# Kernel optimization log

Measured on AMD Instinct MI355X. Metric: run time of the kernel, lower is better.

Reference implementation:

```python
import jax, jax.numpy as jnp
from jax import lax
import numpy as np

B = 4096        # num_batch
NVAR = 120      # 3 * num_legs(4) * horizon(10)
NC = 2 * NVAR   # num_constraints = 240
HID = 1024      # GRU hidden size
RIN = 3 * (NC + NVAR)  # GRU input dim = 1080
MAXITER = 8
RHO = 1.0
REG = 1e-4


def setup_inputs() -> dict:
    key = jax.random.key(0)
    ks = jax.random.split(key, 10)
    # SPD quadratic cost H, linear cost g, inequality constraints C x <= c
    M = jax.random.normal(ks[0], (NVAR, NVAR), jnp.float32)
    H = M @ M.T / NVAR + jnp.eye(NVAR, dtype=jnp.float32)
    g = jax.random.normal(ks[1], (NVAR,), jnp.float32)
    C = 0.1 * jax.random.normal(ks[2], (NC, NVAR), jnp.float32)
    c = jax.random.uniform(ks[3], (NC,), jnp.float32, 0.1, 1.0)
    lamda_init = jax.random.normal(ks[4], (B, NVAR), jnp.float32)
    s_init = jax.random.uniform(ks[5], (B, NC), jnp.float32)
    h_0 = jnp.zeros((B, HID), jnp.float32)
    # GRU cell (torch GRUCell layout: [3*HID, in]) + output head to NC+NVAR
    sc_i = 1.0 / np.sqrt(RIN)
    sc_h = 1.0 / np.sqrt(HID)
    W_ih = sc_i * jax.random.normal(ks[6], (3 * HID, RIN), jnp.float32)
    b_ih = jnp.zeros((3 * HID,), jnp.float32)
    W_hh = sc_h * jax.random.normal(ks[7], (3 * HID, HID), jnp.float32)
    b_hh = jnp.zeros((3 * HID,), jnp.float32)
    W_out = sc_h * jax.random.normal(ks[8], (NC + NVAR, HID), jnp.float32)
    b_out = jnp.zeros((NC + NVAR,), jnp.float32)
    return dict(lamda_init=lamda_init, s_init=s_init, h_0=h_0, H=H, g=g, C=C, c=c,
                W_ih=W_ih, b_ih=b_ih, W_hh=W_hh, b_hh=b_hh, W_out=W_out, b_out=b_out)


def _gru_cell(x, h, W_ih, b_ih, W_hh, b_hh):
    gi = x @ W_ih.T + b_ih
    gh = h @ W_hh.T + b_hh
    i_r, i_z, i_n = jnp.split(gi, 3, axis=1)
    h_r, h_z, h_n = jnp.split(gh, 3, axis=1)
    r = jax.nn.sigmoid(i_r + h_r)
    z = jax.nn.sigmoid(i_z + h_z)
    n = jnp.tanh(i_n + r * h_n)
    return (1.0 - z) * n + z * h


def reference(lamda_init, s_init, h_0, H, g, C, c, W_ih, b_ih, W_hh, b_hh, W_out, b_out):
    I = jnp.eye(NVAR, dtype=H.dtype)
    # ---- init solve (compute_projection_gru preamble) ----
    Q_inv0 = jnp.linalg.pinv(H + REG * I)
    lincost0 = -0.0 * lamda_init + g                 # [B, NVAR]
    xi0 = (-lincost0) @ Q_inv0.T                     # sol = (Qinv @ rhs.T).T
    s0 = jnp.maximum(0.0, -(xi0 @ C.T) + c)
    s0 = 0.0 * s_init + s0                           # s_init = 0*nn + 1*s_
    lam0 = lamda_init
    # ---- constant per-iteration projection matrix (same every iter) ----
    Q_inv = jnp.linalg.pinv(H + RHO * (C.T @ C) + REG * I)

    def step(carry, _):
        s, lam, h = carry
        # compute_feasible_control
        b_aug = c - s                                # [B, NC]
        lincost = -lam + g - RHO * (b_aug @ C)       # [B, NVAR]
        xi = (-lincost) @ Q_inv.T                    # [B, NVAR]
        Axi = xi @ C.T                               # [B, NC]
        s_new = jnp.maximum(0.0, -Axi + c)
        res_vec = Axi - c + s_new
        res_norm = jnp.linalg.norm(res_vec, axis=1)
        lam_new = lam - RHO * (res_vec @ C)
        qp_cost = 0.5 * (xi @ H @ xi.T) + xi @ g     # [B, B] (faithful to source)
        qp_norm = jnp.linalg.norm(qp_cost, axis=1)
        # GRU refinement
        r = jnp.concatenate([s, lam, s_new, lam_new, s_new - s, lam_new - lam], axis=1)
        h_new = _gru_cell(r, h, W_ih, b_ih, W_hh, b_hh)
        out = h_new @ W_out.T + b_out                # [B, NC+NVAR]
        s_fin = jnp.maximum(0.0, s_new + out[:, :NC])
        lam_fin = lam_new + out[:, NC:NC + NVAR]
        fixed = jnp.linalg.norm(lam - lam_fin, axis=1) + jnp.linalg.norm(s - s_fin, axis=1)
        return (s_fin, lam_fin, h_new), (xi, res_norm, fixed, qp_norm)

    (_, _, _), (xis, primal, fixed, qpres) = lax.scan(step, (s0, lam0, h_0), None, length=MAXITER)
    return xis[-1], primal, fixed, qpres
```

## Files before the change

kernel.cpp:

```cpp
#include <hip/hip_runtime.h>
#include <hip/hip_bf16.h>
#include <math.h>

#define NB    4096
#define NV    120
#define NCN   240
#define HIDD  1024
#define RINN  1080
#define NOUTD 360
#define NOUTP 384
#define NITER 8
#define REGEPS 1e-4f
#define NPART 512

#define KCAT 4224
#define HOFF 2176
#define KWC  2112
#define KWO  1024
#define NSTEP_R 34
#define NSTEPS  66

typedef unsigned short u16;
typedef __attribute__((ext_vector_type(8))) short short8v;
typedef __attribute__((ext_vector_type(4))) float f32x4;

__device__ inline u16 f2b(float x) {
    __hip_bfloat16 h = __float2bfloat16(x);
    return __builtin_bit_cast(u16, h);
}
__device__ inline float b2f(u16 u) {
    __hip_bfloat16 h = __builtin_bit_cast(__hip_bfloat16, u);
    return __bfloat162float(h);
}

__device__ inline void gl16(const void* g, void* l) {
    __builtin_amdgcn_global_load_lds(
        (__attribute__((address_space(1))) void*)(void*)g,
        (__attribute__((address_space(3))) void*)l, 16, 0, 0);
}

__global__ void k_buildA(const float* __restrict__ H, const float* __restrict__ C,
                         float* __restrict__ A, float* __restrict__ A0) {
    int i = blockIdx.x;
    int which = blockIdx.y;
    for (int j = threadIdx.x; j < NV; j += blockDim.x) {
        float v = H[i*NV + j] + (i == j ? REGEPS : 0.f);
        if (which == 0) {
            float acc = 0.f;
            for (int k = 0; k < NCN; ++k) acc += C[k*NV + i] * C[k*NV + j];
            A[i*NV + j] = v + acc;
        } else {
            A0[i*NV + j] = v;
        }
    }
}

__global__ void k_buildCT(const float* __restrict__ C, float* __restrict__ CT) {
    int j = blockIdx.x;
    for (int k = threadIdx.x; k < NCN; k += 256)
        CT[(size_t)j * NCN + k] = C[(size_t)k * NV + j];
}

__device__ inline void inv4x4(const float* m, float* inv) {
    float s0 = m[0]*m[5] - m[1]*m[4];
    float s1 = m[0]*m[6] - m[2]*m[4];
    float s2 = m[0]*m[7] - m[3]*m[4];
    float s3 = m[1]*m[6] - m[2]*m[5];
    float s4 = m[1]*m[7] - m[3]*m[5];
    float s5 = m[2]*m[7] - m[3]*m[6];
    float c5 = m[10]*m[15] - m[11]*m[14];
    float c4 = m[9]*m[15] - m[11]*m[13];
    float c3 = m[9]*m[14] - m[10]*m[13];
    float c2 = m[8]*m[15] - m[11]*m[12];
    float c1 = m[8]*m[14] - m[10]*m[12];
    float c0 = m[8]*m[13] - m[9]*m[12];
    float det = s0*c5 - s1*c4 + s2*c3 + s3*c2 - s4*c1 + s5*c0;
    float id = 1.0f / det;
    inv[0]  = ( m[5]*c5 - m[6]*c4 + m[7]*c3) * id;
    inv[1]  = (-m[1]*c5 + m[2]*c4 - m[3]*c3) * id;
    inv[2]  = ( m[13]*s5 - m[14]*s4 + m[15]*s3) * id;
    inv[3]  = (-m[9]*s5 + m[10]*s4 - m[11]*s3) * id;
    inv[4]  = (-m[4]*c5 + m[6]*c2 - m[7]*c1) * id;
    inv[5]  = ( m[0]*c5 - m[2]*c2 + m[3]*c1) * id;
    inv[6]  = (-m[12]*s5 + m[14]*s2 - m[15]*s1) * id;
    inv[7]  = ( m[8]*s5 - m[10]*s2 + m[11]*s1) * id;
    inv[8]  = ( m[4]*c4 - m[5]*c2 + m[7]*c0) * id;
    inv[9]  = (-m[0]*c4 + m[1]*c2 - m[3]*c0) * id;
    inv[10] = ( m[12]*s4 - m[13]*s2 + m[15]*s0) * id;
    inv[11] = (-m[8]*s4 + m[9]*s2 - m[11]*s0) * id;
    inv[12] = (-m[4]*c3 + m[5]*c1 - m[6]*c0) * id;
    inv[13] = ( m[0]*c3 - m[1]*c1 + m[2]*c0) * id;
    inv[14] = (-m[12]*s3 + m[13]*s1 - m[14]*s0) * id;
    inv[15] = ( m[8]*s3 - m[9]*s1 + m[10]*s0) * id;
}

__global__ __launch_bounds__(1024) void k_invert(const float* __restrict__ Ain,
                                                 const float* __restrict__ A0in,
                                                 float* __restrict__ Qi,
                                                 float* __restrict__ Qi0) {
    __shared__ float M[NV][132];
    __shared__ float Rl[4][132];
    __shared__ float Bl[16];
    const float* src = (blockIdx.x == 0) ? Ain : A0in;
    float* dst = (blockIdx.x == 0) ? Qi : Qi0;
    const int t = threadIdx.x;
    for (int idx = t; idx < NV*132; idx += 1024) {
        int i = idx / 132, j = idx - i*132;
        M[i][j] = (j < NV) ? src[i*NV + j] : 0.f;
    }
    __syncthreads();
    const int ty = t >> 5;
    const int g4 = (t & 31) * 4;
    for (int kk = 0; kk < NV; kk += 4) {
        if (ty == 0) {
            float a[16], b[16];
            #pragma unroll
            for (int p = 0; p < 4; ++p) {
                float4 v = *(const float4*)&M[kk + p][kk];
                a[p*4+0] = v.x; a[p*4+1] = v.y; a[p*4+2] = v.z; a[p*4+3] = v.w;
            }
            inv4x4(a, b);
            float4 m0v = *(const float4*)&M[kk+0][g4];
            float4 m1v = *(const float4*)&M[kk+1][g4];
            float4 m2v = *(const float4*)&M[kk+2][g4];
            float4 m3v = *(const float4*)&M[kk+3][g4];
            #pragma unroll
            for (int p = 0; p < 4; ++p) {
                float4 r;
                r.x = b[p*4+0]*m0v.x + b[p*4+1]*m1v.x + b[p*4+2]*m2v.x + b[p*4+3]*m3v.x;
                r.y = b[p*4+0]*m0v.y + b[p*4+1]*m1v.y + b[p*4+2]*m2v.y + b[p*4+3]*m3v.y;
                r.z = b[p*4+0]*m0v.z + b[p*4+1]*m1v.z + b[p*4+2]*m2v.z + b[p*4+3]*m3v.z;
                r.w = b[p*4+0]*m0v.w + b[p*4+1]*m1v.w + b[p*4+2]*m2v.w + b[p*4+3]*m3v.w;
                *(float4*)&Rl[p][g4] = r;
            }
            if (t < 16) Bl[t] = b[t];
        }
        float4 F[4];
        #pragma unroll
        for (int q = 0; q < 4; ++q) {
            int i = ty + 32*q;
            F[q] = (i < NV) ? *(const float4*)&M[i][kk] : float4{0.f,0.f,0.f,0.f};
        }
        __syncthreads();
        #pragma unroll
        for (int q = 0; q < 4; ++q) {
            int i = ty + 32*q;
            if (i < NV) {
                int dp = i - kk;
                bool ispiv = (dp >= 0) && (dp < 4);
                float4 v;
                if (g4 == kk) {
                    if (ispiv) {
                        v = *(const float4*)&Bl[dp*4];
                    } else {
                        v.x = -(F[q].x*Bl[0] + F[q].y*Bl[4] + F[q].z*Bl[8]  + F[q].w*Bl[12]);
                        v.y = -(F[q].x*Bl[1] + F[q].y*Bl[5] + F[q].z*Bl[9]  + F[q].w*Bl[13]);
                        v.z = -(F[q].x*Bl[2] + F[q].y*Bl[6] + F[q].z*Bl[10] + F[q].w*Bl[14]);
                        v.w = -(F[q].x*Bl[3] + F[q].y*Bl[7] + F[q].z*Bl[11] + F[q].w*Bl[15]);
                    }
                } else if (ispiv) {
                    v = *(const float4*)&Rl[dp][g4];
                } else {
                    float4 r0 = *(const float4*)&Rl[0][g4];
                    float4 r1 = *(const float4*)&Rl[1][g4];
                    float4 r2 = *(const float4*)&Rl[2][g4];
                    float4 r3 = *(const float4*)&Rl[3][g4];
                    v = *(const float4*)&M[i][g4];
                    v.x -= F[q].x*r0.x + F[q].y*r1.x + F[q].z*r2.x + F[q].w*r3.x;
                    v.y -= F[q].x*r0.y + F[q].y*r1.y + F[q].z*r2.y + F[q].w*r3.y;
                    v.z -= F[q].x*r0.z + F[q].y*r1.z + F[q].z*r2.z + F[q].w*r3.z;
                    v.w -= F[q].x*r0.w + F[q].y*r1.w + F[q].z*r2.w + F[q].w*r3.w;
                }
                *(float4*)&M[i][g4] = v;
            }
        }
        __syncthreads();
    }
    for (int idx = t; idx < NV*NV; idx += 1024) {
        int i = idx / NV, j = idx - i*NV;
        dst[idx] = M[i][j];
    }
}

__global__ void k_s0(const float* __restrict__ Qi0, const float* __restrict__ g,
                     const float* __restrict__ C, const float* __restrict__ c,
                     float* __restrict__ s0v) {
    __shared__ float xi0[NV];
    int t = threadIdx.x;
    if (t < NV) {
        float a = 0.f;
        for (int j = 0; j < NV; ++j) a += Qi0[t*NV + j] * g[j];
        xi0[t] = -a;
    }
    __syncthreads();
    if (t < NCN) {
        float a = 0.f;
        for (int j = 0; j < NV; ++j) a += C[t*NV + j] * xi0[j];
        s0v[t] = fmaxf(0.f, c[t] - a);
    }
}

__global__ void k_init(const float* __restrict__ s0v, const float* __restrict__ lam0,
                       float* __restrict__ s, float* __restrict__ lam) {
    int b0 = blockIdx.x * 8;
    int t = threadIdx.x;
    for (int idx = t; idx < 8*NCN; idx += 256) {
        int m = idx / NCN, k = idx % NCN;
        s[(size_t)(b0 + m)*NCN + k] = s0v[k];
    }
    for (int idx = t; idx < 8*NV; idx += 256) lam[(size_t)b0*NV + idx] = lam0[(size_t)b0*NV + idx];
}

__global__ void k_packH(const float* __restrict__ h0, u16* __restrict__ act) {
    int n = blockIdx.x;
    size_t base = (size_t)n * KCAT + HOFF;
    for (int k = threadIdx.x; k < HIDD; k += 256) {
        float x = h0[(size_t)n * HIDD + k];
        u16 hi = f2b(x);
        act[base + k] = hi;
        act[base + HIDD + k] = f2b(x - b2f(hi));
    }
}

__global__ void k_packWcat(const float* __restrict__ Wih, const float* __restrict__ Whh,
                           u16* __restrict__ Wc) {
    int n = blockIdx.x;
    size_t base = (size_t)n * KWC;
    for (int k = threadIdx.x; k < 1088; k += 256)
        Wc[base + k] = f2b(k < RINN ? Wih[(size_t)n * RINN + k] : 0.f);
    for (int k = threadIdx.x; k < HIDD; k += 256)
        Wc[base + 1088 + k] = f2b(Whh[(size_t)n * HIDD + k]);
}

__global__ void k_packWo(const float* __restrict__ src, u16* __restrict__ dst) {
    int n = blockIdx.x;
    size_t row = (size_t)n * KWO;
    for (int k = threadIdx.x; k < KWO; k += 256)
        dst[row + k] = f2b(n < NOUTD ? src[(size_t)n * HIDD + k] : 0.f);
}

__device__ inline void write2(u16* __restrict__ act, size_t base, int pos, float x) {
    u16 hi = f2b(x);
    u16 lo = f2b(x - b2f(hi));
    act[base + pos] = hi;
    act[base + 1088 + pos] = lo;
}

__device__ inline float hadd4(float4 v) { return (v.x + v.y) + (v.z + v.w); }

#define XB 8
__global__ __launch_bounds__(512) void k_xiproj(
        const float* __restrict__ s, const float* __restrict__ lam,
        const float* __restrict__ Cg, const float* __restrict__ CTg,
        const float* __restrict__ c,
        const float* __restrict__ g, const float* __restrict__ Qi,
        const float* __restrict__ Hg,
        float* __restrict__ xi, float* __restrict__ Y,
        float* __restrict__ snew, float* __restrict__ lamn,
        u16* __restrict__ act, float* __restrict__ primal,
        double* __restrict__ Gp, double* __restrict__ vp, double* __restrict__ Sp) {
    __shared__ float Msh[31680];
    __shared__ float bd[XB][NCN];
    __shared__ float ul[XB][NV];
    __shared__ float xl[XB][NV];
    __shared__ float resl[XB][NCN];
    __shared__ float wl[XB];
    const int b0 = blockIdx.x * XB;
    const int t = threadIdx.x;

    for (int idx = t; idx < XB*NCN; idx += 512) {
        int m = idx / NCN, k = idx - m*NCN;
        bd[m][k] = c[k] - s[(size_t)(b0 + m)*NCN + k];
    }
    for (int idx = t; idx < NV*NCN; idx += 512) {
        int i = idx / NCN, k = idx - i*NCN;
        Msh[i*244 + k] = CTg[idx];
    }
    __syncthreads();
    if (t < 240) {
        int m = t / 30, jb = t - (t / 30) * 30;
        float4 a0 = {0,0,0,0}, a1 = {0,0,0,0}, a2 = {0,0,0,0}, a3 = {0,0,0,0};
        for (int kg = 0; kg < 60; ++kg) {
            float4 b4 = *(const float4*)&bd[m][kg*4];
            float4 c0 = *(const float4*)&Msh[(jb     ) * 244 + kg*4];
            float4 c1 = *(const float4*)&Msh[(jb + 30) * 244 + kg*4];
            float4 c2 = *(const float4*)&Msh[(jb + 60) * 244 + kg*4];
            float4 c3 = *(const float4*)&Msh[(jb + 90) * 244 + kg*4];
            a0.x += b4.x*c0.x; a0.y += b4.y*c0.y; a0.z += b4.z*c0.z; a0.w += b4.w*c0.w;
            a1.x += b4.x*c1.x; a1.y += b4.y*c1.y; a1.z += b4.z*c1.z; a1.w += b4.w*c1.w;
            a2.x += b4.x*c2.x; a2.y += b4.y*c2.y; a2.z += b4.z*c2.z; a2.w += b4.w*c2.w;
            a3.x += b4.x*c3.x; a3.y += b4.y*c3.y; a3.z += b4.z*c3.z; a3.w += b4.w*c3.w;
        }
        #pragma unroll
        for (int p = 0; p < 4; ++p) {
            int j = jb + 30*p;
            float h = (p == 0) ? hadd4(a0) : (p == 1) ? hadd4(a1) : (p == 2) ? hadd4(a2) : hadd4(a3);
            ul[m][j] = lam[(size_t)(b0 + m)*NV + j] - g[j] + h;
        }
    }
    __syncthreads();
    for (int idx = t; idx < NV*NV; idx += 512) {
        int i = idx / NV, j = idx - i*NV;
        Msh[i*132 + j] = Qi[idx];
        Msh[(120 + i)*132 + j] = Hg[idx];
    }
    __syncthreads();
    if (t < 240) {
        int m = t / 30, ib = t - (t / 30) * 30;
        float4 a0 = {0,0,0,0}, a1 = {0,0,0,0}, a2 = {0,0,0,0}, a3 = {0,0,0,0};
        for (int jg = 0; jg < 30; ++jg) {
            float4 u4 = *(const float4*)&ul[m][jg*4];
            float4 q0 = *(const float4*)&Msh[(ib     ) * 132 + jg*4];
            float4 q1 = *(const float4*)&Msh[(ib + 30) * 132 + jg*4];
            float4 q2 = *(const float4*)&Msh[(ib + 60) * 132 + jg*4];
            float4 q3 = *(const float4*)&Msh[(ib + 90) * 132 + jg*4];
            a0.x += u4.x*q0.x; a0.y += u4.y*q0.y; a0.z += u4.z*q0.z; a0.w += u4.w*q0.w;
            a1.x += u4.x*q1.x; a1.y += u4.y*q1.y; a1.z += u4.z*q1.z; a1.w += u4.w*q1.w;
            a2.x += u4.x*q2.x; a2.y += u4.y*q2.y; a2.z += u4.z*q2.z; a2.w += u4.w*q2.w;
            a3.x += u4.x*q3.x; a3.y += u4.y*q3.y; a3.z += u4.z*q3.z; a3.w += u4.w*q3.w;
        }
        #pragma unroll
        for (int p = 0; p < 4; ++p) {
            int i = ib + 30*p;
            float a = (p == 0) ? hadd4(a0) : (p == 1) ? hadd4(a1) : (p == 2) ? hadd4(a2) : hadd4(a3);
            xl[m][i] = a;
            xi[(size_t)(b0 + m)*NV + i] = a;
        }
    }
    __syncthreads();
    if (t < 240) {
        int m = t / 30, ib = t - (t / 30) * 30;
        float4 a0 = {0,0,0,0}, a1 = {0,0,0,0}, a2 = {0,0,0,0}, a3 = {0,0,0,0};
        for (int jg = 0; jg < 30; ++jg) {
            float4 x4 = *(const float4*)&xl[m][jg*4];
            float4 h0 = *(const float4*)&Msh[(120 + ib     ) * 132 + jg*4];
            float4 h1 = *(const float4*)&Msh[(120 + ib + 30) * 132 + jg*4];
            float4 h2 = *(const float4*)&Msh[(120 + ib + 60) * 132 + jg*4];
            float4 h3 = *(const float4*)&Msh[(120 + ib + 90) * 132 + jg*4];
            a0.x += x4.x*h0.x; a0.y += x4.y*h0.y; a0.z += x4.z*h0.z; a0.w += x4.w*h0.w;
            a1.x += x4.x*h1.x; a1.y += x4.y*h1.y; a1.z += x4.z*h1.z; a1.w += x4.w*h1.w;
            a2.x += x4.x*h2.x; a2.y += x4.y*h2.y; a2.z += x4.z*h2.z; a2.w += x4.w*h2.w;
            a3.x += x4.x*h3.x; a3.y += x4.y*h3.y; a3.z += x4.z*h3.z; a3.w += x4.w*h3.w;
        }
        #pragma unroll
        for (int p = 0; p < 4; ++p) {
            int i = ib + 30*p;
            float a = (p == 0) ? hadd4(a0) : (p == 1) ? hadd4(a1) : (p == 2) ? hadd4(a2) : hadd4(a3);
            Y[(size_t)(b0 + m)*NV + i] = a;
        }
    }
    if (t >= 240 && t < 240 + XB) {
        int m = t - 240;
        float a = 0.f;
        for (int j = 0; j < NV; ++j) a += xl[m][j] * g[j];
        wl[m] = a;
    }
    __syncthreads();
    for (int idx = t; idx < NCN*NV; idx += 512) {
        int k = idx / NV, j = idx - k*NV;
        Msh[k*132 + j] = Cg[idx];
    }
    __syncthreads();
    if (t < 480) {
        int m = t / 60, kb = t - (t / 60) * 60;
        float4 a0 = {0,0,0,0}, a1 = {0,0,0,0}, a2 = {0,0,0,0}, a3 = {0,0,0,0};
        for (int jg = 0; jg < 30; ++jg) {
            float4 x4 = *(const float4*)&xl[m][jg*4];
            float4 c0 = *(const float4*)&Msh[(kb      ) * 132 + jg*4];
            float4 c1 = *(const float4*)&Msh[(kb + 60 ) * 132 + jg*4];
            float4 c2 = *(const float4*)&Msh[(kb + 120) * 132 + jg*4];
            float4 c3 = *(const float4*)&Msh[(kb + 180) * 132 + jg*4];
            a0.x += x4.x*c0.x; a0.y += x4.y*c0.y; a0.z += x4.z*c0.z; a0.w += x4.w*c0.w;
            a1.x += x4.x*c1.x; a1.y += x4.y*c1.y; a1.z += x4.z*c1.z; a1.w += x4.w*c1.w;
            a2.x += x4.x*c2.x; a2.y += x4.y*c2.y; a2.z += x4.z*c2.z; a2.w += x4.w*c2.w;
            a3.x += x4.x*c3.x; a3.y += x4.y*c3.y; a3.z += x4.z*c3.z; a3.w += x4.w*c3.w;
        }
        #pragma unroll
        for (int p = 0; p < 4; ++p) {
            int k = kb + 60*p;
            float a = (p == 0) ? hadd4(a0) : (p == 1) ? hadd4(a1) : (p == 2) ? hadd4(a2) : hadd4(a3);
            float sn = fmaxf(0.f, c[k] - a);
            float rv = a - c[k] + sn;
            resl[m][k] = rv;
            int b = b0 + m;
            snew[(size_t)b*NCN + k] = sn;
            float so = s[(size_t)b*NCN + k];
            size_t base = (size_t)b * KCAT;
            write2(act, base, k, so);
            write2(act, base, 360 + k, sn);
            write2(act, base, 720 + k, sn - so);
        }
    }
    __syncthreads();
    if (t < XB) {
        float a = 0.f;
        for (int k = 0; k < NCN; ++k) a += resl[t][k] * resl[t][k];
        primal[b0 + t] = sqrtf(a);
    }
    for (int idx = t; idx < NV*NCN; idx += 512) {
        int i = idx / NCN, k = idx - i*NCN;
        Msh[i*244 + k] = CTg[idx];
    }
    __syncthreads();
    if (t < 240) {
        int m = t / 30, ib = t - (t / 30) * 30;
        float4 a0 = {0,0,0,0}, a1 = {0,0,0,0}, a2 = {0,0,0,0}, a3 = {0,0,0,0};
        for (int kg = 0; kg < 60; ++kg) {
            float4 r4 = *(const float4*)&resl[m][kg*4];
            float4 c0 = *(const float4*)&Msh[(ib     ) * 244 + kg*4];
            float4 c1 = *(const float4*)&Msh[(ib + 30) * 244 + kg*4];
            float4 c2 = *(const float4*)&Msh[(ib + 60) * 244 + kg*4];
            float4 c3 = *(const float4*)&Msh[(ib + 90) * 244 + kg*4];
            a0.x += r4.x*c0.x; a0.y += r4.y*c0.y; a0.z += r4.z*c0.z; a0.w += r4.w*c0.w;
            a1.x += r4.x*c1.x; a1.y += r4.y*c1.y; a1.z += r4.z*c1.z; a1.w += r4.w*c1.w;
            a2.x += r4.x*c2.x; a2.y += r4.y*c2.y; a2.z += r4.z*c2.z; a2.w += r4.w*c2.w;
            a3.x += r4.x*c3.x; a3.y += r4.y*c3.y; a3.z += r4.z*c3.z; a3.w += r4.w*c3.w;
        }
        #pragma unroll
        for (int p = 0; p < 4; ++p) {
            int i = ib + 30*p;
            float a = (p == 0) ? hadd4(a0) : (p == 1) ? hadd4(a1) : (p == 2) ? hadd4(a2) : hadd4(a3);
            int b = b0 + m;
            float lo = lam[(size_t)b*NV + i];
            float ln = lo - a;
            lamn[(size_t)b*NV + i] = ln;
            size_t base = (size_t)b * KCAT;
            write2(act, base, 240 + i, lo);
            write2(act, base, 600 + i, ln);
            write2(act, base, 960 + i, ln - lo);
        }
    }
    for (int idx = t; idx < XB*8; idx += 512) {
        int m = idx >> 3, k = 1080 + (idx & 7);
        size_t base = (size_t)(b0 + m) * KCAT;
        act[base + k] = 0;
        act[base + 1088 + k] = 0;
    }
    for (int idx = t; idx < NV*NV; idx += 512) {
        int i = idx / NV, j = idx - i*NV;
        double a = 0.0;
        #pragma unroll
        for (int m = 0; m < XB; ++m) a += (double)xl[m][i] * (double)xl[m][j];
        Gp[(size_t)blockIdx.x*NV*NV + idx] = a;
    }
    if (t < NV) {
        double a = 0.0;
        #pragma unroll
        for (int m = 0; m < XB; ++m) a += (double)wl[m] * (double)xl[m][t];
        vp[(size_t)blockIdx.x*NV + t] = a;
    }
    if (t == 0) {
        double a = 0.0;
        #pragma unroll
        for (int m = 0; m < XB; ++m) a += (double)wl[m] * (double)wl[m];
        Sp[blockIdx.x] = a;
    }
}

__global__ void k_qp_red(const double* __restrict__ Gp, const double* __restrict__ vp,
                         const double* __restrict__ Sp,
                         double* __restrict__ G, double* __restrict__ v, double* __restrict__ S) {
    int idx = blockIdx.x * 256 + threadIdx.x;
    if (idx < NV*NV) {
        double a = 0.0;
        for (int p = 0; p < NPART; ++p) a += Gp[(size_t)p*NV*NV + idx];
        G[idx] = a;
    }
    if (idx < NV) {
        double a = 0.0;
        for (int p = 0; p < NPART; ++p) a += vp[(size_t)p*NV + idx];
        v[idx] = a;
    }
    if (idx == 0) {
        double a = 0.0;
        for (int p = 0; p < NPART; ++p) a += Sp[p];
        S[0] = a;
    }
}

__global__ __launch_bounds__(256) void k_tail(
        const float* __restrict__ Yb, const double* __restrict__ G,
        const double* __restrict__ v, const double* __restrict__ S,
        float* __restrict__ qp,
        const float* __restrict__ snew, const float* __restrict__ lamn,
        const float* __restrict__ outb,
        float* __restrict__ s, float* __restrict__ lam,
        float* __restrict__ fx) {
    __shared__ float Yl[16][NV];
    __shared__ double tl[16][NV];
    __shared__ float redS[16][17];
    __shared__ float redL[16][17];
    int b0 = blockIdx.x * 16;
    int t = threadIdx.x;
    for (int idx = t; idx < 16*NV; idx += 256) Yl[idx/NV][idx%NV] = Yb[(size_t)b0*NV + idx];
    __syncthreads();
    for (int idx = t; idx < 16*NV; idx += 256) {
        int m = idx / NV, i = idx % NV;
        double a = 0.0;
        for (int j = 0; j < NV; ++j) a += G[j*NV + i] * (double)Yl[m][j];
        tl[m][i] = a;
    }
    __syncthreads();
    if (t < 16) {
        double a = 0.0, bv = 0.0;
        for (int i = 0; i < NV; ++i) { a += (double)Yl[t][i] * tl[t][i]; bv += (double)Yl[t][i] * v[i]; }
        double q = 0.25 * a + bv + S[0];
        qp[b0 + t] = (float)sqrt(q > 0.0 ? q : 0.0);
    }
    int tm = t / 16;
    int tk = t % 16;
    int b = b0 + tm;
    float ds2 = 0.f, dl2 = 0.f;
    for (int k = tk; k < NCN; k += 16) {
        float o = outb[(size_t)b*NOUTP + k];
        float sf = fmaxf(0.f, snew[(size_t)b*NCN + k] + o);
        float so = s[(size_t)b*NCN + k];
        s[(size_t)b*NCN + k] = sf;
        float d = so - sf;
        ds2 += d * d;
    }
    for (int i = tk; i < NV; i += 16) {
        float o = outb[(size_t)b*NOUTP + NCN + i];
        float lf = lamn[(size_t)b*NV + i] + o;
        float lo = lam[(size_t)b*NV + i];
        lam[(size_t)b*NV + i] = lf;
        float d = lo - lf;
        dl2 += d * d;
    }
    redS[tm][tk] = ds2;
    redL[tm][tk] = dl2;
    __syncthreads();
    if (tk == 0) {
        float a = 0.f, l = 0.f;
        for (int q = 0; q < 16; ++q) { a += redS[tm][q]; l += redL[tm][q]; }
        fx[b] = sqrtf(l) + sqrtf(a);
    }
}

#define GRUF_STEP(NSLOT, BUFI) do {                                              \
    char* Ah_ = lds + (BUFI) * 32768;                                            \
    char* Al_ = Ah_ + 4096;                                                      \
    char* Bb_ = Ah_ + 8192;                                                      \
    const int srow = lane & 15;                                                  \
    const int ksl = lane >> 4;                                                   \
    short8v ah[2], al[2];                                                        \
    _Pragma("unroll")                                                            \
    for (int fm = 0; fm < 2; ++fm) {                                             \
        int rr = wm * 32 + fm * 16 + srow;                                       \
        int off = rr * 64 + ((ksl ^ ((rr >> 1) & 3)) << 4);                      \
        ah[fm] = *(const short8v*)(Ah_ + off);                                   \
        al[fm] = *(const short8v*)(Al_ + off);                                   \
    }                                                                            \
    _Pragma("unroll")                                                            \
    for (int fn = 0; fn < 2; ++fn) {                                             \
        int rb = wn * 32 + fn * 16 + srow;                                       \
        int boff = rb * 64 + ((ksl ^ ((rb >> 1) & 3)) << 4);                     \
        short8v bfr = *(const short8v*)(Bb_ + boff);                             \
        short8v bfz = *(const short8v*)(Bb_ + 8192 + boff);                      \
        short8v bfn = *(const short8v*)(Bb_ + 16384 + boff);                     \
        _Pragma("unroll")                                                        \
        for (int fm = 0; fm < 2; ++fm) {                                         \
            acc[0][fn][fm] = __builtin_amdgcn_mfma_f32_16x16x32_bf16(ah[fm], bfr, acc[0][fn][fm], 0, 0, 0); \
            acc[0][fn][fm] = __builtin_amdgcn_mfma_f32_16x16x32_bf16(al[fm], bfr, acc[0][fn][fm], 0, 0, 0); \
            acc[1][fn][fm] = __builtin_amdgcn_mfma_f32_16x16x32_bf16(ah[fm], bfz, acc[1][fn][fm], 0, 0, 0); \
            acc[1][fn][fm] = __builtin_amdgcn_mfma_f32_16x16x32_bf16(al[fm], bfz, acc[1][fn][fm], 0, 0, 0); \
            acc[NSLOT][fn][fm] = __builtin_amdgcn_mfma_f32_16x16x32_bf16(ah[fm], bfn, acc[NSLOT][fn][fm], 0, 0, 0); \
            acc[NSLOT][fn][fm] = __builtin_amdgcn_mfma_f32_16x16x32_bf16(al[fm], bfn, acc[NSLOT][fn][fm], 0, 0, 0); \
        }                                                                        \
    }                                                                            \
} while (0)

__global__ __launch_bounds__(512) void k_gruf(
        const u16* __restrict__ act,
        const u16* __restrict__ Wc,
        const float* __restrict__ bih, const float* __restrict__ bhh,
        u16* __restrict__ actn) {
    __shared__ char lds[65536];
    const int t = threadIdx.x;
    const int lane = t & 63;
    const int wid = t >> 6;
    const int wm = wid >> 2;
    const int wn = wid & 3;
    const int bid = blockIdx.x;
    const int xcd = bid & 7;
    const int slot = bid >> 3;
    const int m0 = (xcd * 8 + (slot & 7)) * 64;
    const int n0 = (slot >> 3) * 128;

    f32x4 acc[4][2][2];
    #pragma unroll
    for (int i = 0; i < 4; ++i)
        #pragma unroll
        for (int j = 0; j < 2; ++j)
            #pragma unroll
            for (int k = 0; k < 2; ++k) {
                f32x4 z = {0.f, 0.f, 0.f, 0.f};
                acc[i][j][k] = z;
            }

    auto stage = [&](int step, int buf) {
        char* Ah_ = lds + buf * 32768;
        char* Al_ = Ah_ + 4096;
        char* Bb_ = Ah_ + 8192;
        const int hiOff = (step < NSTEP_R) ? step * 32 : step * 32 + 1088;
        const int loOff = hiOff + ((step < NSTEP_R) ? 1088 : 1024);
        const int wOff = step * 32;
        {
            int rr = (wid & 3) * 16 + (lane >> 2);
            int kq = ((lane & 3) ^ ((rr >> 1) & 3)) << 3;
            if (wid < 4)
                gl16(act + (size_t)(m0 + rr) * KCAT + hiOff + kq, Ah_ + (wid & 3) * 1024);
            else
                gl16(act + (size_t)(m0 + rr) * KCAT + loOff + kq, Al_ + (wid & 3) * 1024);
        }
        #pragma unroll
        for (int j = 0; j < 3; ++j) {
            int cb = wid * 3 + j;
            int rbg = cb * 16 + (lane >> 2);
            int kq = ((lane & 3) ^ ((rbg >> 1) & 3)) << 3;
            gl16(Wc + (size_t)((rbg >> 7) * 1024 + n0 + (rbg & 127)) * KWC + wOff + kq,
                 Bb_ + cb * 1024);
        }
    };

    stage(0, 0);
    __syncthreads();
    int cur = 0;
    for (int step = 0; step < NSTEP_R; ++step) {
        stage(step + 1, cur ^ 1);
        GRUF_STEP(2, cur);
        __syncthreads();
        cur ^= 1;
    }
    for (int step = NSTEP_R; step < NSTEPS; ++step) {
        if (step + 1 < NSTEPS) stage(step + 1, cur ^ 1);
        GRUF_STEP(3, cur);
        __syncthreads();
        cur ^= 1;
    }

    #pragma unroll
    for (int fn = 0; fn < 2; ++fn) {
        const int jj = n0 + wn * 32 + fn * 16 + (lane & 15);
        const float bir = bih[jj],        bhr = bhh[jj];
        const float biz = bih[1024 + jj], bhz = bhh[1024 + jj];
        const float bin = bih[2048 + jj], bhn = bhh[2048 + jj];
        #pragma unroll
        for (int fm = 0; fm < 2; ++fm) {
            #pragma unroll
            for (int rg = 0; rg < 4; ++rg) {
                int m = m0 + wm * 32 + fm * 16 + (lane >> 4) * 4 + rg;
                float rz = acc[0][fn][fm][rg];
                float zz = acc[1][fn][fm][rg];
                float inn = acc[2][fn][fm][rg];
                float hnn = acc[3][fn][fm][rg];
                float rgate = 1.f / (1.f + expf(-(rz + bir + bhr)));
                float zgate = 1.f / (1.f + expf(-(zz + biz + bhz)));
                float ngate = tanhf(inn + bin + rgate * (hnn + bhn));
                size_t base = (size_t)m * KCAT + HOFF;
                float hv = b2f(act[base + jj]) + b2f(act[base + HIDD + jj]);
                float hnew = (1.f - zgate) * ngate + zgate * hv;
                u16 nh = f2b(hnew);
                actn[base + jj] = nh;
                actn[base + HIDD + jj] = f2b(hnew - b2f(nh));
            }
        }
    }
}

__global__ __launch_bounds__(512) void k_outp(
        const u16* __restrict__ act, const u16* __restrict__ Wo,
        const float* __restrict__ bo, float* __restrict__ outb) {
    __shared__ char lds[32768];
    const int t = threadIdx.x;
    const int lane = t & 63;
    const int wid = t >> 6;
    const int wm = wid >> 2;
    const int wn = wid & 3;
    const int m0 = blockIdx.x * 64;
    const int n0 = blockIdx.y * 128;
    f32x4 acc[2][2];
    #pragma unroll
    for (int i = 0; i < 2; ++i)
        #pragma unroll
        for (int j = 0; j < 2; ++j) {
            f32x4 z = {0.f, 0.f, 0.f, 0.f};
            acc[i][j] = z;
        }

    auto stage = [&](int step, int buf) {
        char* Ah_ = lds + buf * 16384;
        char* Al_ = Ah_ + 4096;
        char* Bb_ = Ah_ + 8192;
        {
            int rr = (wid & 3) * 16 + (lane >> 2);
            int kq = ((lane & 3) ^ ((rr >> 1) & 3)) << 3;
            if (wid < 4)
                gl16(act + (size_t)(m0 + rr) * KCAT + HOFF + step * 32 + kq,
                     Ah_ + (wid & 3) * 1024);
            else
                gl16(act + (size_t)(m0 + rr) * KCAT + HOFF + HIDD + step * 32 + kq,
                     Al_ + (wid & 3) * 1024);
        }
        {
            int rb = wid * 16 + (lane >> 2);
            int kq = ((lane & 3) ^ ((rb >> 1) & 3)) << 3;
            gl16(Wo + (size_t)(n0 + rb) * KWO + step * 32 + kq, Bb_ + wid * 1024);
        }
    };

    stage(0, 0);
    __syncthreads();
    int cur = 0;
    for (int step = 0; step < 32; ++step) {
        if (step + 1 < 32) stage(step + 1, cur ^ 1);
        {
            char* Ah_ = lds + cur * 16384;
            char* Al_ = Ah_ + 4096;
            char* Bb_ = Ah_ + 8192;
            const int srow = lane & 15;
            const int ksl = lane >> 4;
            short8v ah[2], al[2];
            #pragma unroll
            for (int fm = 0; fm < 2; ++fm) {
                int rr = wm * 32 + fm * 16 + srow;
                int off = rr * 64 + ((ksl ^ ((rr >> 1) & 3)) << 4);
                ah[fm] = *(const short8v*)(Ah_ + off);
                al[fm] = *(const short8v*)(Al_ + off);
            }
            #pragma unroll
            for (int fn = 0; fn < 2; ++fn) {
                int rb = wn * 32 + fn * 16 + srow;
                int boff = rb * 64 + ((ksl ^ ((rb >> 1) & 3)) << 4);
                short8v bf = *(const short8v*)(Bb_ + boff);
                #pragma unroll
                for (int fm = 0; fm < 2; ++fm) {
                    acc[fn][fm] = __builtin_amdgcn_mfma_f32_16x16x32_bf16(ah[fm], bf, acc[fn][fm], 0, 0, 0);
                    acc[fn][fm] = __builtin_amdgcn_mfma_f32_16x16x32_bf16(al[fm], bf, acc[fn][fm], 0, 0, 0);
                }
            }
        }
        __syncthreads();
        cur ^= 1;
    }
    #pragma unroll
    for (int fn = 0; fn < 2; ++fn) {
        int n = n0 + wn * 32 + fn * 16 + (lane & 15);
        if (n < NOUTD) {
            float bb = bo[n];
            #pragma unroll
            for (int fm = 0; fm < 2; ++fm) {
                #pragma unroll
                for (int rg = 0; rg < 4; ++rg) {
                    int m = m0 + wm * 32 + fm * 16 + (lane >> 4) * 4 + rg;
                    outb[(size_t)m * NOUTP + n] = acc[fn][fm][rg] + bb;
                }
            }
        }
    }
}

extern "C" void kernel_launch(void* const* d_in, const int* in_sizes, int n_in,
                              void* d_out, int out_size, void* d_ws, size_t ws_size,
                              hipStream_t stream) {
    const float* lamda_init = (const float*)d_in[0];
    const float* h0    = (const float*)d_in[2];
    const float* H     = (const float*)d_in[3];
    const float* g     = (const float*)d_in[4];
    const float* C     = (const float*)d_in[5];
    const float* c     = (const float*)d_in[6];
    const float* W_ih  = (const float*)d_in[7];
    const float* b_ih  = (const float*)d_in[8];
    const float* W_hh  = (const float*)d_in[9];
    const float* b_hh  = (const float*)d_in[10];
    const float* W_out = (const float*)d_in[11];
    const float* b_out = (const float*)d_in[12];

    float* out    = (float*)d_out;
    float* xi_out = out;
    float* primal = out + (size_t)NB*NV;
    float* fixedo = primal + (size_t)NITER*NB;
    float* qpres  = fixedo + (size_t)NITER*NB;

    char* wp = (char*)d_ws;
    auto alloc = [&](size_t bytes) {
        void* p = (void*)wp;
        wp += (bytes + 255) & ~(size_t)255;
        return p;
    };
    float* Amat  = (float*)alloc(NV*NV*4);
    float* A0m   = (float*)alloc(NV*NV*4);
    float* Qinv  = (float*)alloc(NV*NV*4);
    float* Qinv0 = (float*)alloc(NV*NV*4);
    float* CTg   = (float*)alloc((size_t)NV*NCN*4);
    float* s0v   = (float*)alloc(NCN*4);
    float* sbuf  = (float*)alloc((size_t)NB*NCN*4);
    float* snew  = (float*)alloc((size_t)NB*NCN*4);
    float* lam   = (float*)alloc((size_t)NB*NV*4);
    float* lamn  = (float*)alloc((size_t)NB*NV*4);
    float* xib   = (float*)alloc((size_t)NB*NV*4);
    float* Yb    = (float*)alloc((size_t)NB*NV*4);
    float* outb  = (float*)alloc((size_t)NB*NOUTP*4);
    u16* actA    = (u16*)alloc((size_t)NB*KCAT*2);
    u16* actB    = (u16*)alloc((size_t)NB*KCAT*2);
    u16* Wcat    = (u16*)alloc((size_t)3072*KWC*2);
    u16* Wopk    = (u16*)alloc((size_t)NOUTP*KWO*2);
    double* Gpart = (double*)alloc((size_t)NPART*NV*NV*8);
    double* vpart = (double*)alloc((size_t)NPART*NV*8);
    double* Spart = (double*)alloc(NPART*8);
    double* Gfin  = (double*)alloc(NV*NV*8);
    double* vfin  = (double*)alloc(NV*8);
    double* Sfin  = (double*)alloc(8);

    k_buildA<<<dim3(NV, 2), dim3(128), 0, stream>>>(H, C, Amat, A0m);
    k_buildCT<<<dim3(NV), dim3(256), 0, stream>>>(C, CTg);
    k_invert<<<dim3(2), dim3(1024), 0, stream>>>(Amat, A0m, Qinv, Qinv0);
    k_s0<<<dim3(1), dim3(256), 0, stream>>>(Qinv0, g, C, c, s0v);
    k_init<<<dim3(NB/8), dim3(256), 0, stream>>>(s0v, lamda_init, sbuf, lam);
    k_packWcat<<<dim3(3072), dim3(256), 0, stream>>>(W_ih, W_hh, Wcat);
    k_packWo<<<dim3(NOUTP), dim3(256), 0, stream>>>(W_out, Wopk);
    k_packH<<<dim3(NB), dim3(256), 0, stream>>>(h0, actA);

    u16* hc = actA;
    u16* hn2 = actB;
    for (int it = 0; it < NITER; ++it) {
        k_xiproj<<<dim3(NB/XB), dim3(512), 0, stream>>>(sbuf, lam, C, CTg, c, g, Qinv, H,
                                                        xib, Yb, snew, lamn, hc,
                                                        primal + (size_t)it*NB,
                                                        Gpart, vpart, Spart);
        k_qp_red<<<dim3((NV*NV + 255)/256), dim3(256), 0, stream>>>(Gpart, vpart, Spart, Gfin, vfin, Sfin);
        k_gruf<<<dim3(512), dim3(512), 0, stream>>>(hc, Wcat, b_ih, b_hh, hn2);
        k_outp<<<dim3(64, 3), dim3(512), 0, stream>>>(hn2, Wopk, b_out, outb);
        k_tail<<<dim3(NB/16), dim3(256), 0, stream>>>(Yb, Gfin, vfin, Sfin,
                                                      qpres + (size_t)it*NB,
                                                      snew, lamn, outb, sbuf, lam,
                                                      fixedo + (size_t)it*NB);
        u16* tmp = hc; hc = hn2; hn2 = tmp;
    }
    hipMemcpyAsync(xi_out, xib, (size_t)NB*NV*sizeof(float), hipMemcpyDeviceToDevice, stream);
}
```

Measured before the change: 2.313 ms.

## Split QP Gram partials into separate fp32 kernel and double xiproj batch tile

Moves the per-block Gram matrix, v and S partial accumulation out of k_xiproj into a new k_qp_part kernel that handles 32 rows per block in fp32. Partials drop from 512 to 128, which cuts partial-buffer traffic and the serial loop length in k_qp_red. k_xiproj now processes 16 rows per block, so more threads stay busy, and it reuses the bd buffer as resl to save shared memory. Costs are an extra launch per iteration and fp32 rather than fp64 partial accumulation, which loses some precision in the qp cost.

```diff
diff --git a/kernel.cpp b/kernel.cpp
--- a/kernel.cpp
+++ b/kernel.cpp
@@ -11,7 +11,7 @@
 #define NOUTP 384
 #define NITER 8
 #define REGEPS 1e-4f
-#define NPART 512
+#define NPART 128
 
 #define KCAT 4224
 #define HOFF 2176
@@ -248,25 +248,23 @@
 
 __device__ inline float hadd4(float4 v) { return (v.x + v.y) + (v.z + v.w); }
 
-#define XB 8
+#define XB 16
 __global__ __launch_bounds__(512) void k_xiproj(
         const float* __restrict__ s, const float* __restrict__ lam,
         const float* __restrict__ Cg, const float* __restrict__ CTg,
         const float* __restrict__ c,
         const float* __restrict__ g, const float* __restrict__ Qi,
         const float* __restrict__ Hg,
-        float* __restrict__ xi, float* __restrict__ Y,
+        float* __restrict__ xi, float* __restrict__ Y, float* __restrict__ wv,
         float* __restrict__ snew, float* __restrict__ lamn,
-        u16* __restrict__ act, float* __restrict__ primal,
-        double* __restrict__ Gp, double* __restrict__ vp, double* __restrict__ Sp) {
+        u16* __restrict__ act, float* __restrict__ primal) {
     __shared__ float Msh[31680];
-    __shared__ float bd[XB][NCN];
+    __shared__ float resl[XB][NCN];
     __shared__ float ul[XB][NV];
     __shared__ float xl[XB][NV];
-    __shared__ float resl[XB][NCN];
-    __shared__ float wl[XB];
     const int b0 = blockIdx.x * XB;
     const int t = threadIdx.x;
+    #define bd resl
 
     for (int idx = t; idx < XB*NCN; idx += 512) {
         int m = idx / NCN, k = idx - m*NCN;
@@ -277,7 +275,7 @@
         Msh[i*244 + k] = CTg[idx];
     }
     __syncthreads();
-    if (t < 240) {
+    if (t < 480) {
         int m = t / 30, jb = t - (t / 30) * 30;
         float4 a0 = {0,0,0,0}, a1 = {0,0,0,0}, a2 = {0,0,0,0}, a3 = {0,0,0,0};
         for (int kg = 0; kg < 60; ++kg) {
@@ -305,7 +303,7 @@
         Msh[(120 + i)*132 + j] = Hg[idx];
     }
     __syncthreads();
-    if (t < 240) {
+    if (t < 480) {
         int m = t / 30, ib = t - (t / 30) * 30;
         float4 a0 = {0,0,0,0}, a1 = {0,0,0,0}, a2 = {0,0,0,0}, a3 = {0,0,0,0};
         for (int jg = 0; jg < 30; ++jg) {
@@ -328,7 +326,7 @@
         }
     }
     __syncthreads();
-    if (t < 240) {
+    if (t < 480) {
         int m = t / 30, ib = t - (t / 30) * 30;
         float4 a0 = {0,0,0,0}, a1 = {0,0,0,0}, a2 = {0,0,0,0}, a3 = {0,0,0,0};
         for (int jg = 0; jg < 30; ++jg) {
@@ -349,11 +347,11 @@
             Y[(size_t)(b0 + m)*NV + i] = a;
         }
     }
-    if (t >= 240 && t < 240 + XB) {
-        int m = t - 240;
+    if (t >= 480 && t < 480 + XB) {
+        int m = t - 480;
         float a = 0.f;
         for (int j = 0; j < NV; ++j) a += xl[m][j] * g[j];
-        wl[m] = a;
+        wv[b0 + m] = a;
     }
     __syncthreads();
     for (int idx = t; idx < NCN*NV; idx += 512) {
@@ -361,8 +359,8 @@
         Msh[k*132 + j] = Cg[idx];
     }
     __syncthreads();
-    if (t < 480) {
-        int m = t / 60, kb = t - (t / 60) * 60;
+    for (int s5 = t; s5 < XB*60; s5 += 512) {
+        int m = s5 / 60, kb = s5 - (s5 / 60) * 60;
         float4 a0 = {0,0,0,0}, a1 = {0,0,0,0}, a2 = {0,0,0,0}, a3 = {0,0,0,0};
         for (int jg = 0; jg < 30; ++jg) {
             float4 x4 = *(const float4*)&xl[m][jg*4];
@@ -402,7 +400,7 @@
         Msh[i*244 + k] = CTg[idx];
     }
     __syncthreads();
-    if (t < 240) {
+    if (t < 480) {
         int m = t / 30, ib = t - (t / 30) * 30;
         float4 a0 = {0,0,0,0}, a1 = {0,0,0,0}, a2 = {0,0,0,0}, a3 = {0,0,0,0};
         for (int kg = 0; kg < 60; ++kg) {
@@ -436,44 +434,57 @@
         act[base + k] = 0;
         act[base + 1088 + k] = 0;
     }
-    for (int idx = t; idx < NV*NV; idx += 512) {
-        int i = idx / NV, j = idx - i*NV;
-        double a = 0.0;
-        #pragma unroll
-        for (int m = 0; m < XB; ++m) a += (double)xl[m][i] * (double)xl[m][j];
-        Gp[(size_t)blockIdx.x*NV*NV + idx] = a;
+    #undef bd
+}
+
+__global__ __launch_bounds__(256) void k_qp_part(const float* __restrict__ xi, const float* __restrict__ wv,
+                         float* __restrict__ Gp, float* __restrict__ vp, float* __restrict__ Sp) {
+    __shared__ float xl[32][NV];
+    __shared__ float wl[32];
+    int p = blockIdx.x;
+    int b0 = p * 32;
+    int t = threadIdx.x;
+    for (int idx = t; idx < 32*NV; idx += 256) xl[idx/NV][idx%NV] = xi[(size_t)b0*NV + idx];
+    if (t < 32) wl[t] = wv[b0 + t];
+    __syncthreads();
+    for (int idx = t; idx < NV*NV; idx += 256) {
+        int i = idx / NV, j = idx % NV;
+        float a = 0.f;
+        #pragma unroll
+        for (int m = 0; m < 32; ++m) a += xl[m][i] * xl[m][j];
+        Gp[(size_t)p*NV*NV + idx] = a;
     }
     if (t < NV) {
-        double a = 0.0;
-        #pragma unroll
-        for (int m = 0; m < XB; ++m) a += (double)wl[m] * (double)xl[m][t];
-        vp[(size_t)blockIdx.x*NV + t] = a;
+        float a = 0.f;
+        #pragma unroll
+        for (int m = 0; m < 32; ++m) a += wl[m] * xl[m][t];
+        vp[(size_t)p*NV + t] = a;
     }
     if (t == 0) {
-        double a = 0.0;
-        #pragma unroll
-        for (int m = 0; m < XB; ++m) a += (double)wl[m] * (double)wl[m];
-        Sp[blockIdx.x] = a;
-    }
-}
-
-__global__ void k_qp_red(const double* __restrict__ Gp, const double* __restrict__ vp,
-                         const double* __restrict__ Sp,
+        float a = 0.f;
+        #pragma unroll
+        for (int m = 0; m < 32; ++m) a += wl[m] * wl[m];
+        Sp[p] = a;
+    }
+}
+
+__global__ void k_qp_red(const float* __restrict__ Gp, const float* __restrict__ vp,
+                         const float* __restrict__ Sp,
                          double* __restrict__ G, double* __restrict__ v, double* __restrict__ S) {
     int idx = blockIdx.x * 256 + threadIdx.x;
     if (idx < NV*NV) {
         double a = 0.0;
-        for (int p = 0; p < NPART; ++p) a += Gp[(size_t)p*NV*NV + idx];
+        for (int p = 0; p < NPART; ++p) a += (double)Gp[(size_t)p*NV*NV + idx];
         G[idx] = a;
     }
     if (idx < NV) {
         double a = 0.0;
-        for (int p = 0; p < NPART; ++p) a += vp[(size_t)p*NV + idx];
+        for (int p = 0; p < NPART; ++p) a += (double)vp[(size_t)p*NV + idx];
         v[idx] = a;
     }
     if (idx == 0) {
         double a = 0.0;
-        for (int p = 0; p < NPART; ++p) a += Sp[p];
+        for (int p = 0; p < NPART; ++p) a += (double)Sp[p];
         S[0] = a;
     }
 }
@@ -800,14 +811,15 @@
     float* lamn  = (float*)alloc((size_t)NB*NV*4);
     float* xib   = (float*)alloc((size_t)NB*NV*4);
     float* Yb    = (float*)alloc((size_t)NB*NV*4);
+    float* wb    = (float*)alloc(NB*4);
     float* outb  = (float*)alloc((size_t)NB*NOUTP*4);
     u16* actA    = (u16*)alloc((size_t)NB*KCAT*2);
     u16* actB    = (u16*)alloc((size_t)NB*KCAT*2);
     u16* Wcat    = (u16*)alloc((size_t)3072*KWC*2);
     u16* Wopk    = (u16*)alloc((size_t)NOUTP*KWO*2);
-    double* Gpart = (double*)alloc((size_t)NPART*NV*NV*8);
-    double* vpart = (double*)alloc((size_t)NPART*NV*8);
-    double* Spart = (double*)alloc(NPART*8);
+    float* Gpart = (float*)alloc((size_t)NPART*NV*NV*4);
+    float* vpart = (float*)alloc((size_t)NPART*NV*4);
+    float* Spart = (float*)alloc(NPART*4);
     double* Gfin  = (double*)alloc(NV*NV*8);
     double* vfin  = (double*)alloc(NV*8);
     double* Sfin  = (double*)alloc(8);
@@ -825,9 +837,9 @@
     u16* hn2 = actB;
     for (int it = 0; it < NITER; ++it) {
         k_xiproj<<<dim3(NB/XB), dim3(512), 0, stream>>>(sbuf, lam, C, CTg, c, g, Qinv, H,
-                                                        xib, Yb, snew, lamn, hc,
-                                                        primal + (size_t)it*NB,
-                                                        Gpart, vpart, Spart);
+                                                        xib, Yb, wb, snew, lamn, hc,
+                                                        primal + (size_t)it*NB);
+        k_qp_part<<<dim3(NPART), dim3(256), 0, stream>>>(xib, wb, Gpart, vpart, Spart);
         k_qp_red<<<dim3((NV*NV + 255)/256), dim3(256), 0, stream>>>(Gpart, vpart, Spart, Gfin, vfin, Sfin);
         k_gruf<<<dim3(512), dim3(512), 0, stream>>>(hc, Wcat, b_ih, b_hh, hn2);
         k_outp<<<dim3(64, 3), dim3(512), 0, stream>>>(hn2, Wopk, b_out, outb);
```

Measured after the change: 2.168 ms. 1.07x faster.
